# Kernel optimization log

Hardware: AMD Instinct MI355X
Metric: run time of the kernel (lower is better)

Reference implementation:

```python
import jax, jax.numpy as jnp
import numpy as np

B, Q, C, H, W, E, HID_ATT, HID_MLP, NUM_CLASSES, NUM_LABELS = 8, 64, 512, 16, 16, 512, 128, 512, 14, 64


def setup_inputs() -> dict:
    key = jax.random.key(0)
    ks = jax.random.split(key, 16)
    s = 0.02
    return {
        "feature": jax.random.normal(ks[0], (B, C, H, W), jnp.float32),
        "label_ids": jax.random.randint(ks[1], (B, Q), 0, NUM_LABELS),
        "query_table": jax.random.normal(ks[2], (NUM_LABELS, E), jnp.float32) * s,
        "W_film": jax.random.normal(ks[3], (E, 2 * C), jnp.float32) * s,
        "b_film": jnp.zeros((2 * C,), jnp.float32),
        "W_att_h": jax.random.normal(ks[4], (C, HID_ATT), jnp.float32) * s,
        "b_att_h": jnp.zeros((HID_ATT,), jnp.float32),
        "W_att_f": jax.random.normal(ks[5], (HID_ATT, 1), jnp.float32) * s,
        "b_att_f": jnp.zeros((1,), jnp.float32),
        "W_mlp1": jax.random.normal(ks[6], (C, HID_MLP), jnp.float32) * s,
        "b_mlp1": jnp.zeros((HID_MLP,), jnp.float32),
        "W_mlp2": jax.random.normal(ks[7], (HID_MLP, NUM_CLASSES), jnp.float32) * s,
        "b_mlp2": jnp.zeros((NUM_CLASSES,), jnp.float32),
    }


def gelu(x):
    return jax.nn.gelu(x, approximate=False)  # torch default GELU is exact erf


def reference(feature, label_ids, query_table, W_film, b_film, W_att_h, b_att_h,
              W_att_f, b_att_f, W_mlp1, b_mlp1, W_mlp2, b_mlp2):
    # query embedding lookup: (B, Q, E)
    qe = query_table[label_ids]
    # flatten spatial: (B, HW, C)
    f = feature.reshape(feature.shape[0], feature.shape[1], -1).transpose(0, 2, 1)
    # FiLM params from queries: (B, Q, 2C) -> gamma, beta (B, Q, C)
    gb = jnp.einsum("bqe,ec->bqc", qe, W_film) + b_film
    gamma, beta = jnp.split(gb, 2, axis=-1)
    # FiLM-modulated features: (B, Q, HW, C)
    film = f[:, None, :, :] * gamma[:, :, None, :] + beta[:, :, None, :]
    # local attention MLP -> sigmoid gate (B, Q, HW, 1)
    hidden = gelu(jnp.einsum("bqnc,ch->bqnh", film, W_att_h) + b_att_h)
    attn = jax.nn.sigmoid(jnp.einsum("bqnh,ho->bqno", hidden, W_att_f) + b_att_f)
    # weighted sum pool over HW, normalized by attention mass
    pooled = (attn * film).sum(axis=2) / (attn.sum(axis=2) + 1e-8)  # (B, Q, C)
    # classification MLP
    logits = jnp.einsum("bqh,ho->bqo", gelu(jnp.einsum("bqc,ch->bqh", pooled, W_mlp1) + b_mlp1), W_mlp2) + b_mlp2
    return logits  # (B, Q, NUM_CLASSES)
```

## Files before the change

kernel.cpp:

```cpp
#include <hip/hip_runtime.h>
#include <hip/hip_bf16.h>

#define B_    8
#define Q_    64
#define C_    512
#define HW_   256
#define E_    512
#define HATT_ 128
#define HMLP_ 512
#define NCLS_ 14
#define NLAB_ 64

typedef unsigned short u16;
typedef unsigned int   u32;
typedef __attribute__((ext_vector_type(8))) short short8;
typedef __attribute__((ext_vector_type(4))) float f32x4;


__device__ __forceinline__ float gelu_fast(float x) {
    const float ax = fabsf(x);
    const float t  = __builtin_amdgcn_rcpf(1.0f + 0.3275911f * ax);
    const float p  = t * (0.254829592f +
                     t * (-0.284496736f +
                     t * (1.421413741f +
                     t * (-1.453152027f +
                     t * 1.061405429f))));
    const float e  = __expf(-x * x);
    const float er = copysignf(1.0f - p * e, x);
    return 0.5f * x * (1.0f + er);
}
__device__ __forceinline__ float sigmoid_(float x) {
    return 1.0f / (1.0f + __expf(-x));
}
__device__ __forceinline__ u16 f2bf(float x) {
    u32 u = __float_as_uint(x);
    u32 r = (u + 0x7fffu + ((u >> 16) & 1u)) >> 16;
    return (u16)r;
}
__device__ __forceinline__ float bf2f(u16 u) {
    return __uint_as_float(((u32)u) << 16);
}
__device__ __forceinline__ void gl2lds16(const void* gsrc, void* ldsdst) {
    __builtin_amdgcn_global_load_lds(
        (const __attribute__((address_space(1))) u32*)gsrc,
        (__attribute__((address_space(3))) u32*)ldsdst, 16, 0, 0);
}

__global__ __launch_bounds__(256) void prep_misc(
    const float* __restrict__ qt, const float* __restrict__ W_film,
    const float* __restrict__ feature, const float* __restrict__ W_mlp1,
    const int* __restrict__ label_ids,
    float* __restrict__ GBp, u16* __restrict__ W1bf, u16* __restrict__ fT,
    int* __restrict__ perm) {

    __shared__ __align__(16) char sm[16896];
    const int bid = blockIdx.x, t = threadIdx.x;

    if (bid < 256) {
        float* qrow = (float*)sm;
        const int l = bid >> 2, cq = bid & 3;
        if (t < 128) qrow[t] = qt[l * E_ + cq * 128 + t];
        __syncthreads();
        const float* wp = W_film + (size_t)(cq * 128) * 1024 + t * 4;
        f32x4 a = {0.f, 0.f, 0.f, 0.f};
        #pragma unroll 8
        for (int c = 0; c < 128; ++c) {
            const float4 w = *(const float4*)(wp + (size_t)c * 1024);
            const float q = qrow[c];
            a.x += q * w.x; a.y += q * w.y; a.z += q * w.z; a.w += q * w.w;
        }
        *(f32x4*)&GBp[(size_t)bid * 1024 + t * 4] = a;
    } else if (bid < 512) {
        float (*tile)[65] = (float(*)[65])sm;
        const int bb = bid - 256;
        const int b = bb >> 5, c0 = ((bb >> 2) & 7) * 64, n0 = (bb & 3) * 64;
        const float* fb = feature + (size_t)b * C_ * HW_;
        const int cl = t >> 2, nq = t & 3;
        #pragma unroll
        for (int i = 0; i < 4; ++i) {
            float4 v = *(const float4*)&fb[(c0 + cl) * HW_ + n0 + nq * 16 + i * 4];
            tile[cl][nq * 16 + i * 4 + 0] = v.x;
            tile[cl][nq * 16 + i * 4 + 1] = v.y;
            tile[cl][nq * 16 + i * 4 + 2] = v.z;
            tile[cl][nq * 16 + i * 4 + 3] = v.w;
        }
        __syncthreads();
        const int nl = t >> 2, cqq = t & 3;
        u16 pk[16];
        #pragma unroll
        for (int k = 0; k < 16; ++k) pk[k] = f2bf(tile[cqq * 16 + k][nl]);
        u16* dst = fT + (size_t)(b * HW_ + n0 + nl) * C_ + c0 + cqq * 16;
        *(uint4*)dst       = *(uint4*)pk;
        *(uint4*)(dst + 8) = *(uint4*)(pk + 8);
    } else if (bid < 576) {
        const int b2 = bid - 512;
        #pragma unroll
        for (int k = 0; k < 2; ++k) {
            const int idx = (b2 * 512 + k * 256 + t) * 8;
            float4 v0 = *(const float4*)&W_mlp1[idx];
            float4 v1 = *(const float4*)&W_mlp1[idx + 4];
            u16 pk[8] = {f2bf(v0.x), f2bf(v0.y), f2bf(v0.z), f2bf(v0.w),
                         f2bf(v1.x), f2bf(v1.y), f2bf(v1.z), f2bf(v1.w)};
            *(uint4*)&W1bf[idx] = *(uint4*)pk;
        }
    } else {
        int* cnt = (int*)sm;
        if (t < 64) cnt[t] = 0;
        __syncthreads();
        const int l0 = label_ids[t], l1 = label_ids[t + 256];
        atomicAdd(&cnt[l0], 1);
        atomicAdd(&cnt[l1], 1);
        __syncthreads();
        if (t == 0) {
            int run = 0;
            for (int i = 0; i < 64; ++i) { const int c = cnt[i]; cnt[i] = run; run += c; }
        }
        __syncthreads();
        const int p0 = atomicAdd(&cnt[l0], 1);
        perm[p0] = t | (l0 << 16);
        const int p1 = atomicAdd(&cnt[l1], 1);
        perm[p1] = (t + 256) | (l1 << 16);
    }
}

__global__ __launch_bounds__(256) void prep_wg(
    const float* __restrict__ b_film, const float* __restrict__ W_att_h,
    const float* __restrict__ GBp,
    float* __restrict__ Gl, float* __restrict__ Bl,
    u16* __restrict__ WgT, float* __restrict__ Dlp) {

    __shared__ float g_s[128], b_s[128], dred[256];
    const int bid = blockIdx.x, t = threadIdx.x;
    const int l = bid >> 2, cq = bid & 3;

    if (t < 128) {
        const int c = cq * 128 + t;
        float g = b_film[c], be = b_film[512 + c];
        #pragma unroll
        for (int j = 0; j < 4; ++j) {
            g  += GBp[(size_t)(l * 4 + j) * 1024 + c];
            be += GBp[(size_t)(l * 4 + j) * 1024 + 512 + c];
        }
        g_s[t] = g; b_s[t] = be;
        Gl[l * C_ + c] = g;
        Bl[l * C_ + c] = be;
    }
    __syncthreads();

    const int h = t & 127, ch = t >> 7;
    const int hswz = (h >> 1) & 3;
    float dl = 0.f;
    #pragma unroll
    for (int sl = 0; sl < 2; ++sl) {
        const int ss = cq * 4 + ch * 2 + sl;
        char* dst = (char*)WgT + (size_t)l * 131072 + ss * 8192 + h * 64;
        #pragma unroll
        for (int g = 0; g < 4; ++g) {
            u16 pk[8];
            #pragma unroll
            for (int j = 0; j < 8; ++j) {
                const int cl = ch * 64 + sl * 32 + g * 8 + j;
                const float w = W_att_h[(size_t)(cq * 128 + cl) * HATT_ + h];
                pk[j] = f2bf(g_s[cl] * w);
                dl += b_s[cl] * w;
            }
            *(uint4*)(dst + ((g ^ hswz) * 16)) = *(uint4*)pk;
        }
    }
    dred[t] = dl;
    __syncthreads();
    if (t < 128)
        Dlp[(size_t)(l * 4 + cq) * 128 + t] = dred[t] + dred[128 + t];
}

__global__ __launch_bounds__(512, 4) void attn_gemm(
    const float* __restrict__ W_att_f, const float* __restrict__ b_att_f,
    const float* __restrict__ b_att_h, const float* __restrict__ Dlp,
    const int*   __restrict__ perm,    const u16* __restrict__ WgT,
    const u16*   __restrict__ fT,
    float* __restrict__ pP, float* __restrict__ pA) {

    __shared__ __align__(16) char Ash[2][16384];
    __shared__ __align__(16) char Bsh[2][8192];
    __shared__ float d_s[HATT_];
    __shared__ float wf_s[HATT_];
    __shared__ float attn_part[2][HW_];
    __shared__ float attn_s[HW_];

    const int t = threadIdx.x;
    const int srank = (blockIdx.x & 7) * 64 + (blockIdx.x >> 3);
    const int pe = perm[srank];
    const int bq = pe & 0xffff, l = pe >> 16;
    const int b = bq >> 6;

    if (t < HATT_) {
        d_s[t] = b_att_h[t]
               + Dlp[(size_t)(l * 4 + 0) * 128 + t]
               + Dlp[(size_t)(l * 4 + 1) * 128 + t]
               + Dlp[(size_t)(l * 4 + 2) * 128 + t]
               + Dlp[(size_t)(l * 4 + 3) * 128 + t];
        wf_s[t] = W_att_f[t];
    }

    const u16* fTb = fT + (size_t)b * HW_ * C_;
    const u16* Wl  = WgT + (size_t)l * 65536;

    const int an0 = t >> 2;
    const int asl0 = (t & 3) ^ ((an0 >> 1) & 3);

    #define STAGE(s_) {                                                       \
        _Pragma("unroll")                                                     \
        for (int it = 0; it < 2; ++it)                                        \
            gl2lds16(fTb + (size_t)(it * 128 + an0) * C_ + (s_) * 32          \
                         + asl0 * 8,                                          \
                     &Ash[(s_) & 1][(it * 512 + t) * 16]);                    \
        gl2lds16(Wl + (size_t)(s_) * 4096 + (size_t)t * 8,                    \
                 &Bsh[(s_) & 1][t * 16]);                                     \
    }

    const int lane = t & 63, w = t >> 6;
    const int wm = w >> 1, wc = w & 1;
    const int lr = lane & 15, lk = lane >> 4;

    const f32x4 zero = {0.f, 0.f, 0.f, 0.f};
    f32x4 acc[4][4];
    #pragma unroll
    for (int mi = 0; mi < 4; ++mi)
        #pragma unroll
        for (int ni = 0; ni < 4; ++ni) acc[mi][ni] = zero;

    STAGE(0);
    __syncthreads();

    #pragma unroll 2
    for (int s = 0; s < 16; ++s) {
        if (s < 15) STAGE(s + 1);
        const char* Ab = Ash[s & 1];
        const char* Bb = Bsh[s & 1];
        short8 af[4], bf[4];
        #pragma unroll
        for (int mi = 0; mi < 4; ++mi) {
            const int nl = wm * 64 + mi * 16 + lr;
            af[mi] = *(const short8*)(Ab + nl * 64 + ((lk ^ ((nl >> 1) & 3)) * 16));
        }
        #pragma unroll
        for (int ni = 0; ni < 4; ++ni) {
            const int h = wc * 64 + ni * 16 + lr;
            bf[ni] = *(const short8*)(Bb + h * 64 + ((lk ^ ((h >> 1) & 3)) * 16));
        }
        #pragma unroll
        for (int mi = 0; mi < 4; ++mi)
            #pragma unroll
            for (int ni = 0; ni < 4; ++ni)
                acc[mi][ni] = __builtin_amdgcn_mfma_f32_16x16x32_bf16(
                    af[mi], bf[ni], acc[mi][ni], 0, 0, 0);
        __syncthreads();
    }

    #pragma unroll
    for (int mi = 0; mi < 4; ++mi) {
        #pragma unroll
        for (int j = 0; j < 4; ++j) {
            float sum = 0.f;
            #pragma unroll
            for (int ni = 0; ni < 4; ++ni) {
                const int h = wc * 64 + ni * 16 + lr;
                sum += gelu_fast(acc[mi][ni][j] + d_s[h]) * wf_s[h];
            }
            sum += __shfl_xor(sum, 1);
            sum += __shfl_xor(sum, 2);
            sum += __shfl_xor(sum, 4);
            sum += __shfl_xor(sum, 8);
            if (lr == 0) attn_part[wc][wm * 64 + mi * 16 + lk * 4 + j] = sum;
        }
    }
    __syncthreads();
    if (t < HW_)
        attn_s[t] = sigmoid_(attn_part[0][t] + attn_part[1][t] + b_att_f[0]);
    __syncthreads();
    if (t < 64) {
        float a = attn_s[t] + attn_s[t + 64] + attn_s[t + 128] + attn_s[t + 192];
        #pragma unroll
        for (int m = 1; m < 64; m <<= 1) a += __shfl_xor(a, m);
        if (t == 0) pA[bq] = a;
    }

    float* pred = (float*)Ash;
    {
        const int ng = t >> 7, cb = (t & 127) * 4;
        const u16* fp = fTb + cb;
        f32x4 p = zero;
        #pragma unroll 8
        for (int n = ng * 64; n < ng * 64 + 64; ++n) {
            const uint2 v = *(const uint2*)(fp + (size_t)n * C_);
            const float a = attn_s[n];
            p.x += a * __uint_as_float(v.x << 16);
            p.y += a * __uint_as_float(v.x & 0xffff0000u);
            p.z += a * __uint_as_float(v.y << 16);
            p.w += a * __uint_as_float(v.y & 0xffff0000u);
        }
        *(f32x4*)&pred[ng * 512 + cb] = p;
    }
    __syncthreads();
    pP[(size_t)bq * C_ + t] = pred[t] + pred[512 + t] + pred[1024 + t] + pred[1536 + t];
}

__global__ __launch_bounds__(512) void mlp_head(
    const int*   __restrict__ label_ids,
    const float* __restrict__ Gl, const float* __restrict__ Bl,
    const float* __restrict__ b_mlp1, const float* __restrict__ W_mlp2,
    const float* __restrict__ b_mlp2, const float* __restrict__ pP,
    const float* __restrict__ pA,     const u16* __restrict__ W1bf,
    float* __restrict__ out) {

    __shared__ float pooled_s[2][C_];
    __shared__ float zred[2][2][HMLP_];
    __shared__ float z_s[2][HMLP_];
    __shared__ float red_s[32 * NCLS_];

    const int t = threadIdx.x;
    const int bq0 = blockIdx.x * 2;

    {
        const int bqi = t >> 8, cc = (t & 255) * 2;
        const int bq = bq0 + bqi, l = label_ids[bq];
        const float A = pA[bq];
        const float inv = 1.0f / (A + 1e-8f);
        #pragma unroll
        for (int i = 0; i < 2; ++i) {
            const int c = cc + i;
            const float p = pP[(size_t)bq * C_ + c];
            pooled_s[bqi][c] = (Gl[l * C_ + c] * p + Bl[l * C_ + c] * A) * inv;
        }
    }
    __syncthreads();

    {
        const int hp = t & 255, cg = t >> 8;
        float z00 = 0.f, z01 = 0.f, z10 = 0.f, z11 = 0.f;
        const u16* wp = W1bf + hp * 2;
        #pragma unroll 8
        for (int c = cg * 256; c < cg * 256 + 256; ++c) {
            const u32 v = *(const u32*)(wp + (size_t)c * HMLP_);
            const float w0 = __uint_as_float(v << 16);
            const float w1 = __uint_as_float(v & 0xffff0000u);
            const float pa = pooled_s[0][c], pb = pooled_s[1][c];
            z00 += pa * w0; z01 += pa * w1;
            z10 += pb * w0; z11 += pb * w1;
        }
        float2 a0 = {z00, z01}, a1 = {z10, z11};
        *(float2*)&zred[cg][0][hp * 2] = a0;
        *(float2*)&zred[cg][1][hp * 2] = a1;
    }
    __syncthreads();
    {
        const int bqi = t >> 8, h2 = (t & 255) * 2;
        #pragma unroll
        for (int i = 0; i < 2; ++i) {
            const int h = h2 + i;
            z_s[bqi][h] = gelu_fast(zred[0][bqi][h] + zred[1][bqi][h] + b_mlp1[h]);
        }
    }
    __syncthreads();

    #pragma unroll
    for (int bqi = 0; bqi < 2; ++bqi) {
        if (t < 448) {
            const int o = t % 14, seg = t / 14;
            float s = 0.f;
            #pragma unroll
            for (int k = 0; k < 16; ++k) {
                const int h = seg * 16 + k;
                s += z_s[bqi][h] * W_mlp2[h * NCLS_ + o];
            }
            red_s[seg * NCLS_ + o] = s;
        }
        __syncthreads();
        if (t < NCLS_) {
            float s = b_mlp2[t];
            #pragma unroll
            for (int seg = 0; seg < 32; ++seg) s += red_s[seg * NCLS_ + t];
            out[(bq0 + bqi) * NCLS_ + t] = s;
        }
        __syncthreads();
    }
}

extern "C" void kernel_launch(void* const* d_in, const int* in_sizes, int n_in,
                              void* d_out, int out_size, void* d_ws, size_t ws_size,
                              hipStream_t stream) {
    const float* feature   = (const float*)d_in[0];
    const int*   label_ids = (const int*)  d_in[1];
    const float* qt        = (const float*)d_in[2];
    const float* W_film    = (const float*)d_in[3];
    const float* b_film    = (const float*)d_in[4];
    const float* W_att_h   = (const float*)d_in[5];
    const float* b_att_h   = (const float*)d_in[6];
    const float* W_att_f   = (const float*)d_in[7];
    const float* b_att_f   = (const float*)d_in[8];
    const float* W_mlp1    = (const float*)d_in[9];
    const float* b_mlp1    = (const float*)d_in[10];
    const float* W_mlp2    = (const float*)d_in[11];
    const float* b_mlp2    = (const float*)d_in[12];
    float* out = (float*)d_out;

    char* wsb   = (char*)d_ws;
    float* GBp  = (float*)wsb;
    float* pP   = (float*)wsb;
    float* pA   = (float*)(wsb + 1048576);
    int*   perm = (int*)  (wsb + 1050624);
    float* Dlp  = (float*)(wsb + 1052672);
    float* Gl   = (float*)(wsb + 1183744);
    float* Bl   = (float*)(wsb + 1314816);
    u16*   W1bf = (u16*)  (wsb + 1445888);
    u16*   fTp  = (u16*)  (wsb + 1970176);
    u16*   WgT  = (u16*)  (wsb + 4067328);

    hipLaunchKernelGGL(prep_misc, dim3(577), dim3(256), 0, stream,
                       qt, W_film, feature, W_mlp1, label_ids,
                       GBp, W1bf, fTp, perm);
    hipLaunchKernelGGL(prep_wg, dim3(256), dim3(256), 0, stream,
                       b_film, W_att_h, GBp, Gl, Bl, WgT, Dlp);
    hipLaunchKernelGGL(attn_gemm, dim3(512), dim3(512), 0, stream,
                       W_att_f, b_att_f, b_att_h, Dlp, perm, WgT, fTp, pP, pA);
    hipLaunchKernelGGL(mlp_head, dim3(256), dim3(512), 0, stream,
                       label_ids, Gl, Bl, b_mlp1, W_mlp2, b_mlp2,
                       pP, pA, W1bf, out);
}
```

Measured before the change: 68.77 us.

## Split attention GEMM over spatial halves and rebalance prep kernels

The attention GEMM now launches 1024 blocks of 256 threads, each handling half of the 256 spatial positions for one query. The partial pooled sums are written as bf16 and the attention masses per half, then combined in the MLP head. The prep stages are rearranged: the FiLM projection runs alone first, and the feature transpose, W1 conversion, permutation and gated-weight build are merged into one kernel. This aims for more parallelism and better load balance, at the cost of duplicated weight loads per block and bf16 rounding of the partial sums.

```diff
diff --git a/kernel.cpp b/kernel.cpp
--- a/kernel.cpp
+++ b/kernel.cpp
@@ -46,34 +46,39 @@
         (__attribute__((address_space(3))) u32*)ldsdst, 16, 0, 0);
 }
 
-__global__ __launch_bounds__(256) void prep_misc(
+__global__ __launch_bounds__(256) void prep_gbp(
     const float* __restrict__ qt, const float* __restrict__ W_film,
+    float* __restrict__ GBp) {
+    __shared__ float qrow[128];
+    const int bid = blockIdx.x, t = threadIdx.x;
+    const int l = bid >> 2, cq = bid & 3;
+    if (t < 128) qrow[t] = qt[l * E_ + cq * 128 + t];
+    __syncthreads();
+    const float* wp = W_film + (size_t)(cq * 128) * 1024 + t * 4;
+    f32x4 a = {0.f, 0.f, 0.f, 0.f};
+    #pragma unroll 8
+    for (int c = 0; c < 128; ++c) {
+        const float4 w = *(const float4*)(wp + (size_t)c * 1024);
+        const float q = qrow[c];
+        a.x += q * w.x; a.y += q * w.y; a.z += q * w.z; a.w += q * w.w;
+    }
+    *(f32x4*)&GBp[(size_t)bid * 1024 + t * 4] = a;
+}
+
+__global__ __launch_bounds__(256) void prep_rest(
     const float* __restrict__ feature, const float* __restrict__ W_mlp1,
-    const int* __restrict__ label_ids,
-    float* __restrict__ GBp, u16* __restrict__ W1bf, u16* __restrict__ fT,
-    int* __restrict__ perm) {
+    const int* __restrict__ label_ids, const float* __restrict__ b_film,
+    const float* __restrict__ W_att_h, const float* __restrict__ GBp,
+    u16* __restrict__ W1bf, u16* __restrict__ fT, int* __restrict__ perm,
+    float* __restrict__ Gl, float* __restrict__ Bl,
+    u16* __restrict__ WgT, float* __restrict__ Dlp) {
 
     __shared__ __align__(16) char sm[16896];
     const int bid = blockIdx.x, t = threadIdx.x;
 
     if (bid < 256) {
-        float* qrow = (float*)sm;
-        const int l = bid >> 2, cq = bid & 3;
-        if (t < 128) qrow[t] = qt[l * E_ + cq * 128 + t];
-        __syncthreads();
-        const float* wp = W_film + (size_t)(cq * 128) * 1024 + t * 4;
-        f32x4 a = {0.f, 0.f, 0.f, 0.f};
-        #pragma unroll 8
-        for (int c = 0; c < 128; ++c) {
-            const float4 w = *(const float4*)(wp + (size_t)c * 1024);
-            const float q = qrow[c];
-            a.x += q * w.x; a.y += q * w.y; a.z += q * w.z; a.w += q * w.w;
-        }
-        *(f32x4*)&GBp[(size_t)bid * 1024 + t * 4] = a;
-    } else if (bid < 512) {
         float (*tile)[65] = (float(*)[65])sm;
-        const int bb = bid - 256;
-        const int b = bb >> 5, c0 = ((bb >> 2) & 7) * 64, n0 = (bb & 3) * 64;
+        const int b = bid >> 5, c0 = ((bid >> 2) & 7) * 64, n0 = (bid & 3) * 64;
         const float* fb = feature + (size_t)b * C_ * HW_;
         const int cl = t >> 2, nq = t & 3;
         #pragma unroll
@@ -92,8 +97,8 @@
         u16* dst = fT + (size_t)(b * HW_ + n0 + nl) * C_ + c0 + cqq * 16;
         *(uint4*)dst       = *(uint4*)pk;
         *(uint4*)(dst + 8) = *(uint4*)(pk + 8);
-    } else if (bid < 576) {
-        const int b2 = bid - 512;
+    } else if (bid < 320) {
+        const int b2 = bid - 256;
         #pragma unroll
         for (int k = 0; k < 2; ++k) {
             const int idx = (b2 * 512 + k * 256 + t) * 8;
@@ -103,7 +108,7 @@
                          f2bf(v1.x), f2bf(v1.y), f2bf(v1.z), f2bf(v1.w)};
             *(uint4*)&W1bf[idx] = *(uint4*)pk;
         }
-    } else {
+    } else if (bid == 320) {
         int* cnt = (int*)sm;
         if (t < 64) cnt[t] = 0;
         __syncthreads();
@@ -120,76 +125,73 @@
         perm[p0] = t | (l0 << 16);
         const int p1 = atomicAdd(&cnt[l1], 1);
         perm[p1] = (t + 256) | (l1 << 16);
-    }
-}
-
-__global__ __launch_bounds__(256) void prep_wg(
-    const float* __restrict__ b_film, const float* __restrict__ W_att_h,
-    const float* __restrict__ GBp,
-    float* __restrict__ Gl, float* __restrict__ Bl,
-    u16* __restrict__ WgT, float* __restrict__ Dlp) {
-
-    __shared__ float g_s[128], b_s[128], dred[256];
-    const int bid = blockIdx.x, t = threadIdx.x;
-    const int l = bid >> 2, cq = bid & 3;
-
-    if (t < 128) {
-        const int c = cq * 128 + t;
-        float g = b_film[c], be = b_film[512 + c];
-        #pragma unroll
-        for (int j = 0; j < 4; ++j) {
-            g  += GBp[(size_t)(l * 4 + j) * 1024 + c];
-            be += GBp[(size_t)(l * 4 + j) * 1024 + 512 + c];
-        }
-        g_s[t] = g; b_s[t] = be;
-        Gl[l * C_ + c] = g;
-        Bl[l * C_ + c] = be;
-    }
-    __syncthreads();
-
-    const int h = t & 127, ch = t >> 7;
-    const int hswz = (h >> 1) & 3;
-    float dl = 0.f;
-    #pragma unroll
-    for (int sl = 0; sl < 2; ++sl) {
-        const int ss = cq * 4 + ch * 2 + sl;
-        char* dst = (char*)WgT + (size_t)l * 131072 + ss * 8192 + h * 64;
-        #pragma unroll
-        for (int g = 0; g < 4; ++g) {
-            u16 pk[8];
-            #pragma unroll
-            for (int j = 0; j < 8; ++j) {
-                const int cl = ch * 64 + sl * 32 + g * 8 + j;
-                const float w = W_att_h[(size_t)(cq * 128 + cl) * HATT_ + h];
-                pk[j] = f2bf(g_s[cl] * w);
-                dl += b_s[cl] * w;
+    } else {
+        float* g_s  = (float*)sm;
+        float* b_s  = g_s + 128;
+        float* dred = b_s + 128;
+        const int wb = bid - 321;
+        const int l = wb >> 2, cq = wb & 3;
+
+        if (t < 128) {
+            const int c = cq * 128 + t;
+            float g = b_film[c], be = b_film[512 + c];
+            #pragma unroll
+            for (int j = 0; j < 4; ++j) {
+                g  += GBp[(size_t)(l * 4 + j) * 1024 + c];
+                be += GBp[(size_t)(l * 4 + j) * 1024 + 512 + c];
             }
-            *(uint4*)(dst + ((g ^ hswz) * 16)) = *(uint4*)pk;
-        }
-    }
-    dred[t] = dl;
-    __syncthreads();
-    if (t < 128)
-        Dlp[(size_t)(l * 4 + cq) * 128 + t] = dred[t] + dred[128 + t];
-}
-
-__global__ __launch_bounds__(512, 4) void attn_gemm(
+            g_s[t] = g; b_s[t] = be;
+            Gl[l * C_ + c] = g;
+            Bl[l * C_ + c] = be;
+        }
+        __syncthreads();
+
+        const int h = t & 127, ch = t >> 7;
+        const int hswz = (h >> 1) & 3;
+        float dl = 0.f;
+        #pragma unroll
+        for (int sl = 0; sl < 2; ++sl) {
+            const int ss = cq * 4 + ch * 2 + sl;
+            char* dst = (char*)WgT + (size_t)l * 131072 + ss * 8192 + h * 64;
+            #pragma unroll
+            for (int g = 0; g < 4; ++g) {
+                u16 pk[8];
+                #pragma unroll
+                for (int j = 0; j < 8; ++j) {
+                    const int cl = ch * 64 + sl * 32 + g * 8 + j;
+                    const float w = W_att_h[(size_t)(cq * 128 + cl) * HATT_ + h];
+                    pk[j] = f2bf(g_s[cl] * w);
+                    dl += b_s[cl] * w;
+                }
+                *(uint4*)(dst + ((g ^ hswz) * 16)) = *(uint4*)pk;
+            }
+        }
+        dred[t] = dl;
+        __syncthreads();
+        if (t < 128)
+            Dlp[(size_t)(l * 4 + cq) * 128 + t] = dred[t] + dred[128 + t];
+    }
+}
+
+__global__ __launch_bounds__(256, 4) void attn_gemm(
     const float* __restrict__ W_att_f, const float* __restrict__ b_att_f,
     const float* __restrict__ b_att_h, const float* __restrict__ Dlp,
     const int*   __restrict__ perm,    const u16* __restrict__ WgT,
     const u16*   __restrict__ fT,
-    float* __restrict__ pP, float* __restrict__ pA) {
-
-    __shared__ __align__(16) char Ash[2][16384];
+    u16* __restrict__ pPb, float* __restrict__ pA) {
+
+    __shared__ __align__(16) char Ash[2][8192];
     __shared__ __align__(16) char Bsh[2][8192];
     __shared__ float d_s[HATT_];
     __shared__ float wf_s[HATT_];
-    __shared__ float attn_part[2][HW_];
-    __shared__ float attn_s[HW_];
+    __shared__ float attn_part[2][128];
+    __shared__ float attn_s[128];
 
     const int t = threadIdx.x;
-    const int srank = (blockIdx.x & 7) * 64 + (blockIdx.x >> 3);
-    const int pe = perm[srank];
+    const int idx = blockIdx.x;
+    const int srank2 = (idx & 7) * 128 + (idx >> 3);
+    const int r = srank2 >> 1, nh = srank2 & 1;
+    const int pe = perm[r];
     const int bq = pe & 0xffff, l = pe >> 16;
     const int b = bq >> 6;
 
@@ -202,20 +204,22 @@
         wf_s[t] = W_att_f[t];
     }
 
-    const u16* fTb = fT + (size_t)b * HW_ * C_;
+    const u16* fTb = fT + (size_t)b * HW_ * C_ + (size_t)nh * 128 * C_;
     const u16* Wl  = WgT + (size_t)l * 65536;
 
-    const int an0 = t >> 2;
+    const int an0  = t >> 2;
     const int asl0 = (t & 3) ^ ((an0 >> 1) & 3);
 
     #define STAGE(s_) {                                                       \
         _Pragma("unroll")                                                     \
         for (int it = 0; it < 2; ++it)                                        \
-            gl2lds16(fTb + (size_t)(it * 128 + an0) * C_ + (s_) * 32          \
+            gl2lds16(fTb + (size_t)(it * 64 + an0) * C_ + (s_) * 32           \
                          + asl0 * 8,                                          \
-                     &Ash[(s_) & 1][(it * 512 + t) * 16]);                    \
-        gl2lds16(Wl + (size_t)(s_) * 4096 + (size_t)t * 8,                    \
-                 &Bsh[(s_) & 1][t * 16]);                                     \
+                     &Ash[(s_) & 1][(it * 256 + t) * 16]);                    \
+        _Pragma("unroll")                                                     \
+        for (int it = 0; it < 2; ++it)                                        \
+            gl2lds16(Wl + (size_t)(s_) * 4096 + (size_t)(it * 256 + t) * 8,   \
+                     &Bsh[(s_) & 1][(it * 256 + t) * 16]);                    \
     }
 
     const int lane = t & 63, w = t >> 6;
@@ -275,14 +279,14 @@
         }
     }
     __syncthreads();
-    if (t < HW_)
+    if (t < 128)
         attn_s[t] = sigmoid_(attn_part[0][t] + attn_part[1][t] + b_att_f[0]);
     __syncthreads();
     if (t < 64) {
-        float a = attn_s[t] + attn_s[t + 64] + attn_s[t + 128] + attn_s[t + 192];
+        float a = attn_s[t] + attn_s[t + 64];
         #pragma unroll
         for (int m = 1; m < 64; m <<= 1) a += __shfl_xor(a, m);
-        if (t == 0) pA[bq] = a;
+        if (t == 0) pA[bq * 2 + nh] = a;
     }
 
     float* pred = (float*)Ash;
@@ -302,14 +306,20 @@
         *(f32x4*)&pred[ng * 512 + cb] = p;
     }
     __syncthreads();
-    pP[(size_t)bq * C_ + t] = pred[t] + pred[512 + t] + pred[1024 + t] + pred[1536 + t];
+    {
+        const int c0 = t * 2;
+        const float v0 = pred[c0]     + pred[512 + c0];
+        const float v1 = pred[c0 + 1] + pred[512 + c0 + 1];
+        u16 pk[2] = {f2bf(v0), f2bf(v1)};
+        *(u32*)&pPb[(size_t)(bq * 2 + nh) * 512 + c0] = *(u32*)pk;
+    }
 }
 
 __global__ __launch_bounds__(512) void mlp_head(
     const int*   __restrict__ label_ids,
     const float* __restrict__ Gl, const float* __restrict__ Bl,
     const float* __restrict__ b_mlp1, const float* __restrict__ W_mlp2,
-    const float* __restrict__ b_mlp2, const float* __restrict__ pP,
+    const float* __restrict__ b_mlp2, const u16* __restrict__ pPb,
     const float* __restrict__ pA,     const u16* __restrict__ W1bf,
     float* __restrict__ out) {
 
@@ -324,12 +334,13 @@
     {
         const int bqi = t >> 8, cc = (t & 255) * 2;
         const int bq = bq0 + bqi, l = label_ids[bq];
-        const float A = pA[bq];
+        const float A = pA[bq * 2] + pA[bq * 2 + 1];
         const float inv = 1.0f / (A + 1e-8f);
         #pragma unroll
         for (int i = 0; i < 2; ++i) {
             const int c = cc + i;
-            const float p = pP[(size_t)bq * C_ + c];
+            const float p = bf2f(pPb[(size_t)(bq * 2) * 512 + c])
+                          + bf2f(pPb[(size_t)(bq * 2 + 1) * 512 + c]);
             pooled_s[bqi][c] = (Gl[l * C_ + c] * p + Bl[l * C_ + c] * A) * inv;
         }
     }
@@ -406,24 +417,24 @@
 
     char* wsb   = (char*)d_ws;
     float* GBp  = (float*)wsb;
-    float* pP   = (float*)wsb;
+    u16*   pPb  = (u16*)  wsb;
     float* pA   = (float*)(wsb + 1048576);
-    int*   perm = (int*)  (wsb + 1050624);
-    float* Dlp  = (float*)(wsb + 1052672);
-    float* Gl   = (float*)(wsb + 1183744);
-    float* Bl   = (float*)(wsb + 1314816);
-    u16*   W1bf = (u16*)  (wsb + 1445888);
-    u16*   fTp  = (u16*)  (wsb + 1970176);
-    u16*   WgT  = (u16*)  (wsb + 4067328);
-
-    hipLaunchKernelGGL(prep_misc, dim3(577), dim3(256), 0, stream,
-                       qt, W_film, feature, W_mlp1, label_ids,
-                       GBp, W1bf, fTp, perm);
-    hipLaunchKernelGGL(prep_wg, dim3(256), dim3(256), 0, stream,
-                       b_film, W_att_h, GBp, Gl, Bl, WgT, Dlp);
-    hipLaunchKernelGGL(attn_gemm, dim3(512), dim3(512), 0, stream,
-                       W_att_f, b_att_f, b_att_h, Dlp, perm, WgT, fTp, pP, pA);
+    int*   perm = (int*)  (wsb + 1052672);
+    float* Dlp  = (float*)(wsb + 1054720);
+    float* Gl   = (float*)(wsb + 1185792);
+    float* Bl   = (float*)(wsb + 1316864);
+    u16*   W1bf = (u16*)  (wsb + 1447936);
+    u16*   fTp  = (u16*)  (wsb + 1972224);
+    u16*   WgT  = (u16*)  (wsb + 4069376);
+
+    hipLaunchKernelGGL(prep_gbp, dim3(256), dim3(256), 0, stream,
+                       qt, W_film, GBp);
+    hipLaunchKernelGGL(prep_rest, dim3(577), dim3(256), 0, stream,
+                       feature, W_mlp1, label_ids, b_film, W_att_h, GBp,
+                       W1bf, fTp, perm, Gl, Bl, WgT, Dlp);
+    hipLaunchKernelGGL(attn_gemm, dim3(1024), dim3(256), 0, stream,
+                       W_att_f, b_att_f, b_att_h, Dlp, perm, WgT, fTp, pPb, pA);
     hipLaunchKernelGGL(mlp_head, dim3(256), dim3(512), 0, stream,
                        label_ids, Gl, Bl, b_mlp1, W_mlp2, b_mlp2,
-                       pP, pA, W1bf, out);
-}
+                       pPb, pA, W1bf, out);
+}
```

Measured after the change: 68.50 us. No clear change (-0.4%).
